# Performance work log

Measured on AMD Instinct MI355X. Metric: run time of the kernel, lower is better.

The kernel has to match this reference:

```python
import jax, jax.numpy as jnp
import numpy as np
import math

D_MODEL = 1024
N_HEADS = 16
D_FF = 4096
EPS = 1e-6
NEG = -1e9


def layer_norm(x, gamma, beta):
    # Faithful to torch: std with Bessel correction (ddof=1), eps added to std.
    mean = jnp.mean(x, axis=-1, keepdims=True)
    std = jnp.std(x, axis=-1, keepdims=True, ddof=1)
    return gamma * ((x - mean) / (std + EPS)) + beta


def mha(x_q, x_kv, wq, bq, wk, bk, wv, bv, wo, bo, mask):
    B, Sq, D = x_q.shape
    Sk = x_kv.shape[1]
    dk = D // N_HEADS
    q = (x_q @ wq + bq).reshape(B, Sq, N_HEADS, dk).transpose(0, 2, 1, 3)
    k = (x_kv @ wk + bk).reshape(B, Sk, N_HEADS, dk).transpose(0, 2, 1, 3)
    v = (x_kv @ wv + bv).reshape(B, Sk, N_HEADS, dk).transpose(0, 2, 1, 3)
    scores = jnp.einsum('bhqd,bhkd->bhqk', q, k) / math.sqrt(dk)
    scores = jnp.where(mask == 0, NEG, scores)
    attn = jax.nn.softmax(scores, axis=-1)
    out = jnp.einsum('bhqk,bhkd->bhqd', attn, v)
    out = out.transpose(0, 2, 1, 3).reshape(B, Sq, D)
    return out @ wo + bo


def setup_inputs() -> dict:
    key = jax.random.key(0)
    ks = jax.random.split(key, 24)
    B, S, D = 2, 2048, D_MODEL
    sc = 0.02
    lin = lambda k, i, o: jax.random.normal(k, (i, o), jnp.float32) * sc
    inp = {
        'x': jax.random.normal(ks[0], (B, S, D), jnp.float32),
        'encoder_output': jax.random.normal(ks[1], (B, S, D), jnp.float32),
        'src_mask': jnp.ones((1, 1, 1, S), jnp.int32),
        'tgt_mask': jnp.tril(jnp.ones((S, S), jnp.int32))[None, None],
        # self-attention params
        'sa_wq': lin(ks[2], D, D), 'sa_bq': jnp.zeros((D,), jnp.float32),
        'sa_wk': lin(ks[3], D, D), 'sa_bk': jnp.zeros((D,), jnp.float32),
        'sa_wv': lin(ks[4], D, D), 'sa_bv': jnp.zeros((D,), jnp.float32),
        'sa_wo': lin(ks[5], D, D), 'sa_bo': jnp.zeros((D,), jnp.float32),
        # cross-attention params
        'ca_wq': lin(ks[6], D, D), 'ca_bq': jnp.zeros((D,), jnp.float32),
        'ca_wk': lin(ks[7], D, D), 'ca_bk': jnp.zeros((D,), jnp.float32),
        'ca_wv': lin(ks[8], D, D), 'ca_bv': jnp.zeros((D,), jnp.float32),
        'ca_wo': lin(ks[9], D, D), 'ca_bo': jnp.zeros((D,), jnp.float32),
        # feed-forward params
        'ff_w1': lin(ks[10], D, D_FF), 'ff_b1': jnp.zeros((D_FF,), jnp.float32),
        'ff_w2': lin(ks[11], D_FF, D), 'ff_b2': jnp.zeros((D,), jnp.float32),
        # layer norms (3 residual connections)
        'n1_g': jnp.ones((D,), jnp.float32), 'n1_b': jnp.zeros((D,), jnp.float32),
        'n2_g': jnp.ones((D,), jnp.float32), 'n2_b': jnp.zeros((D,), jnp.float32),
        'n3_g': jnp.ones((D,), jnp.float32), 'n3_b': jnp.zeros((D,), jnp.float32),
    }
    return inp


def reference(x, encoder_output, src_mask, tgt_mask,
              sa_wq, sa_bq, sa_wk, sa_bk, sa_wv, sa_bv, sa_wo, sa_bo,
              ca_wq, ca_bq, ca_wk, ca_bk, ca_wv, ca_bv, ca_wo, ca_bo,
              ff_w1, ff_b1, ff_w2, ff_b2,
              n1_g, n1_b, n2_g, n2_b, n3_g, n3_b):
    # Pre-norm residual block 1: self-attention (dropout=0 -> identity)
    h = layer_norm(x, n1_g, n1_b)
    x = x + mha(h, h, sa_wq, sa_bq, sa_wk, sa_bk, sa_wv, sa_bv, sa_wo, sa_bo, tgt_mask)
    # Block 2: cross-attention over encoder output
    h = layer_norm(x, n2_g, n2_b)
    x = x + mha(h, encoder_output, ca_wq, ca_bq, ca_wk, ca_bk, ca_wv, ca_bv, ca_wo, ca_bo, src_mask)
    # Block 3: feed-forward
    h = layer_norm(x, n3_g, n3_b)
    ff = jax.nn.relu(h @ ff_w1 + ff_b1) @ ff_w2 + ff_b2
    return x + ff
```

## Files before the change

### kernel.cpp

```cpp
#include <hip/hip_runtime.h>

typedef short short8 __attribute__((ext_vector_type(8)));
typedef float f32x4 __attribute__((ext_vector_type(4)));

#define SEQ 2048
#define QSCALE 0.18033688011112042f
#define PSHIFT 20.0f
#define EXP2(x) __builtin_amdgcn_exp2f(x)

#define GLDS(g, l) __builtin_amdgcn_global_load_lds( \
    (const __attribute__((address_space(1))) unsigned int*)(g), \
    (__attribute__((address_space(3))) unsigned int*)(l), 16, 0, 0)

__device__ __forceinline__ unsigned short f2bf(float f) {
    unsigned int u = __builtin_bit_cast(unsigned int, f);
    unsigned int r = (u + 0x7fffu + ((u >> 16) & 1u)) >> 16;
    return (unsigned short)r;
}

__global__ __launch_bounds__(256)
void wtrans8_kernel(const float* w0, const float* w1, const float* w2, const float* w3,
                    const float* w4, const float* w5, const float* w6, const float* w7,
                    unsigned short* __restrict__ outbase)
{
    const float* Ws[8] = {w0, w1, w2, w3, w4, w5, w6, w7};
    const float* __restrict__ W = Ws[blockIdx.z];
    unsigned short* __restrict__ Wt = outbase + (size_t)blockIdx.z * 1024 * 1024;
    __shared__ float t[32][33];
    const int tx = threadIdx.x & 31;
    const int ty = threadIdx.x >> 5;
    const int nb = blockIdx.x * 32;
    const int kb = blockIdx.y * 32;
#pragma unroll
    for (int i = 0; i < 4; i++)
        t[ty + i * 8][tx] = W[(size_t)(kb + ty + i * 8) * 1024 + nb + tx];
    __syncthreads();
#pragma unroll
    for (int i = 0; i < 4; i++)
        Wt[(size_t)(nb + ty + i * 8) * 1024 + kb + tx] = f2bf(t[tx][ty + i * 8]);
}

__global__ __launch_bounds__(256)
void wtrans_kernel(const float* __restrict__ W, unsigned short* __restrict__ Wt,
                   int Kd, int Nd)
{
    __shared__ float t[32][33];
    const int tx = threadIdx.x & 31;
    const int ty = threadIdx.x >> 5;
    const int nb = blockIdx.x * 32;
    const int kb = blockIdx.y * 32;
#pragma unroll
    for (int i = 0; i < 4; i++)
        t[ty + i * 8][tx] = W[(size_t)(kb + ty + i * 8) * Nd + nb + tx];
    __syncthreads();
#pragma unroll
    for (int i = 0; i < 4; i++)
        Wt[(size_t)(nb + ty + i * 8) * Kd + kb + tx] = f2bf(t[tx][ty + i * 8]);
}

__global__ __launch_bounds__(256)
void cvt_kernel(const float* __restrict__ in, unsigned short* __restrict__ out, int n)
{
    int i = (blockIdx.x * 256 + threadIdx.x) * 4;
    if (i < n) {
        float4 v = *(const float4*)(in + i);
        ushort4 o;
        o.x = f2bf(v.x); o.y = f2bf(v.y); o.z = f2bf(v.z); o.w = f2bf(v.w);
        *(ushort4*)(out + i) = o;
    }
}

__global__ __launch_bounds__(256)
void ln_kernel(const float* __restrict__ x, const float* __restrict__ g,
               const float* __restrict__ bb, unsigned short* __restrict__ out)
{
    const int D = 1024;
    const int row = blockIdx.x;
    const float* xr = x + (size_t)row * D;
    float v[4];
    float s = 0.f, ss = 0.f;
#pragma unroll
    for (int i = 0; i < 4; i++) {
        v[i] = xr[threadIdx.x + i * 256];
        s += v[i];
        ss += v[i] * v[i];
    }
#pragma unroll
    for (int off = 1; off < 64; off <<= 1) {
        s  += __shfl_xor(s,  off, 64);
        ss += __shfl_xor(ss, off, 64);
    }
    __shared__ float red[8];
    const int wave = threadIdx.x >> 6;
    if ((threadIdx.x & 63) == 0) { red[wave] = s; red[4 + wave] = ss; }
    __syncthreads();
    s  = red[0] + red[1] + red[2] + red[3];
    ss = red[4] + red[5] + red[6] + red[7];
    float mean = s / D;
    float var  = fmaxf((ss - s * mean) / (D - 1), 0.f);
    float inv  = 1.f / (sqrtf(var) + 1e-6f);
#pragma unroll
    for (int i = 0; i < 4; i++) {
        int c = threadIdx.x + i * 256;
        out[(size_t)row * D + c] = f2bf(g[c] * (v[i] - mean) * inv + bb[c]);
    }
}

template <int MODE>
__global__ __launch_bounds__(256)
void gemm_kernel(const unsigned short* __restrict__ A,
                 const unsigned short* __restrict__ A2,
                 const unsigned short* __restrict__ Wt,
                 const float* __restrict__ b0,
                 const float* __restrict__ b1,
                 const float* __restrict__ b2,
                 unsigned short* __restrict__ o0,
                 unsigned short* __restrict__ o1,
                 unsigned short* __restrict__ o2,
                 int M, int N, int K)
{
    __shared__ unsigned short As[128 * 32];
    __shared__ unsigned short Bs[128 * 32];
    const int tid  = threadIdx.x;
    const int lane = tid & 63;
    const int wv   = tid >> 6;
    const int quad = lane >> 4;
    const int l16  = lane & 15;
    const int m0 = blockIdx.y * 128;
    const int n0 = blockIdx.x * 128;
    const int wm = (wv >> 1) << 6;
    const int wn = (wv & 1) << 6;
    const int sect = (MODE == 1) ? (n0 >> 10) : 0;
    const unsigned short* Asel = (MODE == 1 && sect != 0) ? A2 : A;

    const int srow0 = wv * 32 + (lane >> 2);
    const int srow1 = srow0 + 16;
    const int scol8 = (lane & 3) * 8;
    unsigned short* asw0 = &As[(wv * 2 + 0) * 512];
    unsigned short* asw1 = &As[(wv * 2 + 1) * 512];
    unsigned short* bsw0 = &Bs[(wv * 2 + 0) * 512];
    unsigned short* bsw1 = &Bs[(wv * 2 + 1) * 512];
    const unsigned short* Ag0 = Asel + (size_t)(m0 + srow0) * K + scol8;
    const unsigned short* Ag1 = Asel + (size_t)(m0 + srow1) * K + scol8;
    const unsigned short* Bg0 = Wt   + (size_t)(n0 + srow0) * K + scol8;
    const unsigned short* Bg1 = Wt   + (size_t)(n0 + srow1) * K + scol8;

    f32x4 acc[4][4];
#pragma unroll
    for (int i = 0; i < 4; i++)
#pragma unroll
        for (int j = 0; j < 4; j++) acc[i][j] = f32x4{0.f, 0.f, 0.f, 0.f};

    for (int k0 = 0; k0 < K; k0 += 32) {
        GLDS(Ag0 + k0, asw0);
        GLDS(Ag1 + k0, asw1);
        GLDS(Bg0 + k0, bsw0);
        GLDS(Bg1 + k0, bsw1);
        __syncthreads();
        short8 af[4], bfr[4];
#pragma unroll
        for (int i = 0; i < 4; i++)
            af[i] = *(const short8*)(&As[(wm + i * 16 + l16) * 32 + quad * 8]);
#pragma unroll
        for (int i = 0; i < 4; i++)
            bfr[i] = *(const short8*)(&Bs[(wn + i * 16 + l16) * 32 + quad * 8]);
#pragma unroll
        for (int mi = 0; mi < 4; mi++)
#pragma unroll
            for (int ni = 0; ni < 4; ni++)
                acc[mi][ni] = __builtin_amdgcn_mfma_f32_16x16x32_bf16(
                    af[mi], bfr[ni], acc[mi][ni], 0, 0, 0);
        __syncthreads();
    }

    if (MODE == 1) {
        const float* bias = (sect == 0) ? b0 : ((sect == 1) ? b1 : b2);
        if (sect == 2) {
#pragma unroll
            for (int mi = 0; mi < 4; mi++)
#pragma unroll
                for (int ni = 0; ni < 4; ni++) {
                    const int cc = (n0 + wn + ni * 16 + l16) & 1023;
                    const int h = cc >> 6, d = cc & 63;
                    const float bv = bias[cc];
                    const int rowg = m0 + wm + mi * 16 + quad * 4;
                    const int b = rowg >> 11, s = rowg & 2047;
                    ushort4 o4;
                    o4.x = f2bf(acc[mi][ni][0] + bv);
                    o4.y = f2bf(acc[mi][ni][1] + bv);
                    o4.z = f2bf(acc[mi][ni][2] + bv);
                    o4.w = f2bf(acc[mi][ni][3] + bv);
                    *(ushort4*)&o2[((size_t)(b * 16 + h) * 64 + d) * SEQ + s] = o4;
                }
        } else {
            unsigned short* dst = (sect == 0) ? o0 : o1;
            const float scl = (sect == 0) ? QSCALE : 1.0f;
#pragma unroll
            for (int mi = 0; mi < 4; mi++)
#pragma unroll
                for (int ni = 0; ni < 4; ni++) {
                    const int cc = (n0 + wn + ni * 16 + l16) & 1023;
                    const int h = cc >> 6, d = cc & 63;
                    const float bv = bias[cc];
#pragma unroll
                    for (int r = 0; r < 4; r++) {
                        const int rowg = m0 + wm + mi * 16 + quad * 4 + r;
                        const int b = rowg >> 11, s = rowg & 2047;
                        float v = (acc[mi][ni][r] + bv) * scl;
                        dst[((size_t)(b * 16 + h) * SEQ + s) * 64 + d] = f2bf(v);
                    }
                }
        }
    } else {
#pragma unroll
        for (int mi = 0; mi < 4; mi++)
#pragma unroll
            for (int ni = 0; ni < 4; ni++) {
                const int colg = n0 + wn + ni * 16 + l16;
                const float bv = b0[colg];
#pragma unroll
                for (int r = 0; r < 4; r++) {
                    const int rowg = m0 + wm + mi * 16 + quad * 4 + r;
                    float v = acc[mi][ni][r] + bv;
                    o0[(size_t)rowg * N + colg] = f2bf(fmaxf(v, 0.f));
                }
            }
    }
}

__global__ __launch_bounds__(256, 1)
void gemm_db_kernel(const unsigned short* __restrict__ A,
                    const unsigned short* __restrict__ Wt,
                    const float* __restrict__ b0,
                    const float* __restrict__ res,
                    float* __restrict__ outf,
                    int M, int N, int K, int cm, int cn)
{
    __shared__ unsigned short As[2][128 * 64];
    __shared__ unsigned short Bs[2][128 * 64];
    const int tid  = threadIdx.x;
    const int lane = tid & 63;
    const int wv   = tid >> 6;
    const int quad = lane >> 4;
    const int l16  = lane & 15;
    const int NX  = gridDim.x;
    const int id  = blockIdx.y * NX + blockIdx.x;
    const int xcd = id & 7, slot = id >> 3;
    const int ngx = NX / cn;
    const int rg = xcd / ngx, cg = xcd - rg * ngx;
    const int m0 = (rg * cm + (slot % cm)) * 128;
    const int n0 = (cg * cn + (slot / cm)) * 128;
    const int wm = (wv >> 1) << 6;
    const int wn = (wv & 1) << 6;

    const int rsub = lane >> 3;
    const int cu8  = ((lane & 7) ^ rsub) * 8;
    const unsigned short* Ag = A  + (size_t)(m0 + wv * 32 + rsub) * K + cu8;
    const unsigned short* Bg = Wt + (size_t)(n0 + wv * 32 + rsub) * K + cu8;

    f32x4 acc[4][4];
#pragma unroll
    for (int i = 0; i < 4; i++)
#pragma unroll
        for (int j = 0; j < 4; j++) acc[i][j] = f32x4{0.f, 0.f, 0.f, 0.f};

    const int NT = K >> 6;

    short8 ar[4], br[4];

    auto ldregs = [&](int t) {
        const int kb = t << 6;
#pragma unroll
        for (int r = 0; r < 4; r++) {
            ar[r] = *(const short8*)(Ag + (size_t)(r * 8) * K + kb);
            br[r] = *(const short8*)(Bg + (size_t)(r * 8) * K + kb);
        }
    };
    auto wrlds = [&](int b) {
#pragma unroll
        for (int r = 0; r < 4; r++) {
            *(short8*)&As[b][(wv * 4 + r) * 512 + lane * 8] = ar[r];
            *(short8*)&Bs[b][(wv * 4 + r) * 512 + lane * 8] = br[r];
        }
    };

    ldregs(0);
    asm volatile("s_waitcnt vmcnt(0)" ::: "memory");
    wrlds(0);
    asm volatile("s_waitcnt lgkmcnt(0)" ::: "memory");
    __builtin_amdgcn_s_barrier();

    for (int i = 0; i < NT; i++) {
        const int cur = i & 1;
        if (i + 1 < NT) ldregs(i + 1);

#pragma unroll
        for (int ks = 0; ks < 2; ks++) {
            short8 af[4], bfr[4];
#pragma unroll
            for (int mi = 0; mi < 4; mi++)
                af[mi] = *(const short8*)(&As[cur][(wm + mi * 16 + l16) * 64 +
                             (((ks * 4 + quad) ^ (l16 & 7)) * 8)]);
#pragma unroll
            for (int ni = 0; ni < 4; ni++)
                bfr[ni] = *(const short8*)(&Bs[cur][(wn + ni * 16 + l16) * 64 +
                             (((ks * 4 + quad) ^ (l16 & 7)) * 8)]);
#pragma unroll
            for (int mi = 0; mi < 4; mi++)
#pragma unroll
                for (int ni = 0; ni < 4; ni++)
                    acc[mi][ni] = __builtin_amdgcn_mfma_f32_16x16x32_bf16(
                        af[mi], bfr[ni], acc[mi][ni], 0, 0, 0);
        }

        if (i + 1 < NT) {
            asm volatile("s_waitcnt vmcnt(0)" ::: "memory");
            wrlds(cur ^ 1);
            asm volatile("s_waitcnt lgkmcnt(0)" ::: "memory");
            __builtin_amdgcn_s_barrier();
        }
    }

#pragma unroll
    for (int mi = 0; mi < 4; mi++)
#pragma unroll
        for (int ni = 0; ni < 4; ni++) {
            const int colg = n0 + wn + ni * 16 + l16;
            const float bv = b0[colg];
#pragma unroll
            for (int r = 0; r < 4; r++) {
                const int rowg = m0 + wm + mi * 16 + quad * 4 + r;
                outf[(size_t)rowg * N + colg] =
                    acc[mi][ni][r] + bv + res[(size_t)rowg * N + colg];
            }
        }
}

template <bool CAUSAL>
__global__ __launch_bounds__(256, 2)
void attn4_kernel(const unsigned short* __restrict__ Q,
                  const unsigned short* __restrict__ K,
                  const unsigned short* __restrict__ VT,
                  unsigned short* __restrict__ O)
{
    __shared__ unsigned short Ks[128 * 72];
    __shared__ unsigned short Vt[64 * 136];
    __shared__ unsigned short Ps[4][32 * 136];
    __shared__ float sumS[4][32];
    const int tid  = threadIdx.x;
    const int lane = tid & 63;
    const int wave = tid >> 6;
    const int quad = lane >> 4;
    const int l16  = lane & 15;
    const int bh = blockIdx.y;
    const int qb = (CAUSAL && (bh & 16)) ? (15 - (int)blockIdx.x) : (int)blockIdx.x;
    const int q0 = qb * 128;
    const size_t baseK = (size_t)bh * SEQ * 64;
    const size_t baseV = (size_t)bh * 64 * SEQ;

    short8 aq[2][2];
#pragma unroll
    for (int qs = 0; qs < 2; qs++) {
        const unsigned short* qp =
            Q + baseK + (size_t)(q0 + wave * 32 + qs * 16 + l16) * 64 + quad * 8;
        aq[qs][0] = *(const short8*)(qp);
        aq[qs][1] = *(const short8*)(qp + 32);
    }
    f32x4 acc[4][2];
#pragma unroll
    for (int i = 0; i < 4; i++)
#pragma unroll
        for (int j = 0; j < 2; j++) acc[i][j] = f32x4{0.f, 0.f, 0.f, 0.f};
    float lsum[2][4] = {{0.f, 0.f, 0.f, 0.f}, {0.f, 0.f, 0.f, 0.f}};

    const int nkb = CAUSAL ? (qb + 1) : (SEQ / 128);
    const int krow = tid >> 1;
    const int kc   = (tid & 1) * 32;
    const int vrow = tid >> 2;
    const int vc   = (tid & 3) * 32;
    const unsigned short* kg = K  + baseK + (size_t)krow * 64 + kc;
    const unsigned short* vg = VT + baseV + (size_t)vrow * SEQ + vc;

    short8 kr0 = *(const short8*)(kg),      kr1 = *(const short8*)(kg + 8);
    short8 kr2 = *(const short8*)(kg + 16), kr3 = *(const short8*)(kg + 24);
    short8 vr0 = *(const short8*)(vg),      vr1 = *(const short8*)(vg + 8);
    short8 vr2 = *(const short8*)(vg + 16), vr3 = *(const short8*)(vg + 24);

    for (int kb = 0; kb < nkb; kb++) {
        __syncthreads();
        *(short8*)&Ks[krow * 72 + kc]      = kr0;
        *(short8*)&Ks[krow * 72 + kc + 8]  = kr1;
        *(short8*)&Ks[krow * 72 + kc + 16] = kr2;
        *(short8*)&Ks[krow * 72 + kc + 24] = kr3;
        *(short8*)&Vt[vrow * 136 + vc]      = vr0;
        *(short8*)&Vt[vrow * 136 + vc + 8]  = vr1;
        *(short8*)&Vt[vrow * 136 + vc + 16] = vr2;
        *(short8*)&Vt[vrow * 136 + vc + 24] = vr3;
        if (kb + 1 < nkb) {
            const unsigned short* kg2 = kg + (size_t)(kb + 1) * 128 * 64;
            const unsigned short* vg2 = vg + (size_t)(kb + 1) * 128;
            kr0 = *(const short8*)(kg2);      kr1 = *(const short8*)(kg2 + 8);
            kr2 = *(const short8*)(kg2 + 16); kr3 = *(const short8*)(kg2 + 24);
            vr0 = *(const short8*)(vg2);      vr1 = *(const short8*)(vg2 + 8);
            vr2 = *(const short8*)(vg2 + 16); vr3 = *(const short8*)(vg2 + 24);
        }
        __syncthreads();

        const bool maskTile = CAUSAL && (kb == nkb - 1);
#pragma unroll
        for (int qs = 0; qs < 2; qs++) {
            f32x4 scf[8];
#pragma unroll
            for (int nt = 0; nt < 8; nt++) {
                f32x4 z = f32x4{0.f, 0.f, 0.f, 0.f};
#pragma unroll
                for (int c = 0; c < 2; c++) {
                    short8 bk = *(const short8*)(&Ks[(nt * 16 + l16) * 72 + c * 32 + quad * 8]);
                    z = __builtin_amdgcn_mfma_f32_16x16x32_bf16(aq[qs][c], bk, z, 0, 0, 0);
                }
                scf[nt] = z;
            }
            if (maskTile) {
                const int qg = q0 + wave * 32 + qs * 16 + quad * 4;
                const int k0 = kb * 128;
#pragma unroll
                for (int nt = 0; nt < 8; nt++) {
                    const int kg_ = k0 + nt * 16 + l16;
#pragma unroll
                    for (int r = 0; r < 4; r++)
                        if (kg_ > qg + r) scf[nt][r] = -1e9f;
                }
            }
#pragma unroll
            for (int nt = 0; nt < 8; nt++)
#pragma unroll
                for (int r = 0; r < 4; r++) {
                    float pv = EXP2(scf[nt][r] - PSHIFT);
                    lsum[qs][r] += pv;
                    Ps[wave][(qs * 16 + quad * 4 + r) * 136 +
                             ((nt * 16 + l16) ^ (quad * 8))] = f2bf(pv);
                }
        }
        const int pswz = 8 * (quad ^ ((l16 >> 2) & 3));
#pragma unroll
        for (int c = 0; c < 4; c++) {
            short8 av[4];
#pragma unroll
            for (int mi = 0; mi < 4; mi++)
                av[mi] = *(const short8*)(&Vt[(mi * 16 + l16) * 136 + c * 32 + quad * 8]);
#pragma unroll
            for (int qs = 0; qs < 2; qs++) {
                short8 bp = *(const short8*)(&Ps[wave][(qs * 16 + l16) * 136 + c * 32 + pswz]);
#pragma unroll
                for (int mi = 0; mi < 4; mi++)
                    acc[mi][qs] = __builtin_amdgcn_mfma_f32_16x16x32_bf16(av[mi], bp, acc[mi][qs], 0, 0, 0);
            }
        }
    }
#pragma unroll
    for (int qs = 0; qs < 2; qs++)
#pragma unroll
        for (int r = 0; r < 4; r++) {
#pragma unroll
            for (int off = 1; off < 16; off <<= 1)
                lsum[qs][r] += __shfl_xor(lsum[qs][r], off, 64);
        }
    if (l16 == 0) {
#pragma unroll
        for (int qs = 0; qs < 2; qs++)
#pragma unroll
            for (int r = 0; r < 4; r++)
                sumS[wave][qs * 16 + quad * 4 + r] = lsum[qs][r];
    }
    __syncthreads();
    const int b = bh >> 4, h = bh & 15;
#pragma unroll
    for (int qs = 0; qs < 2; qs++) {
        const float rcpL = 1.f / sumS[wave][qs * 16 + l16];
        const int qg = q0 + wave * 32 + qs * 16 + l16;
#pragma unroll
        for (int mi = 0; mi < 4; mi++) {
            ushort4 o4;
            o4.x = f2bf(acc[mi][qs][0] * rcpL);
            o4.y = f2bf(acc[mi][qs][1] * rcpL);
            o4.z = f2bf(acc[mi][qs][2] * rcpL);
            o4.w = f2bf(acc[mi][qs][3] * rcpL);
            *(ushort4*)&O[(size_t)(b * SEQ + qg) * 1024 + h * 64 + mi * 16 + quad * 4] = o4;
        }
    }
}

extern "C" void kernel_launch(void* const* d_in, const int* in_sizes, int n_in,
                              void* d_out, int out_size, void* d_ws, size_t ws_size,
                              hipStream_t stream)
{
    (void)in_sizes; (void)n_in; (void)out_size; (void)ws_size;
    const int B = 2, S = SEQ, D = 1024, DFF = 4096;
    const int M = B * S;

    const float* x     = (const float*)d_in[0];
    const float* enc   = (const float*)d_in[1];
    const float* sa_wq = (const float*)d_in[4],  *sa_bq = (const float*)d_in[5];
    const float* sa_wk = (const float*)d_in[6],  *sa_bk = (const float*)d_in[7];
    const float* sa_wv = (const float*)d_in[8],  *sa_bv = (const float*)d_in[9];
    const float* sa_wo = (const float*)d_in[10], *sa_bo = (const float*)d_in[11];
    const float* ca_wq = (const float*)d_in[12], *ca_bq = (const float*)d_in[13];
    const float* ca_wk = (const float*)d_in[14], *ca_bk = (const float*)d_in[15];
    const float* ca_wv = (const float*)d_in[16], *ca_bv = (const float*)d_in[17];
    const float* ca_wo = (const float*)d_in[18], *ca_bo = (const float*)d_in[19];
    const float* ff_w1 = (const float*)d_in[20], *ff_b1 = (const float*)d_in[21];
    const float* ff_w2 = (const float*)d_in[22], *ff_b2 = (const float*)d_in[23];
    const float* n1_g  = (const float*)d_in[24], *n1_b = (const float*)d_in[25];
    const float* n2_g  = (const float*)d_in[26], *n2_b = (const float*)d_in[27];
    const float* n3_g  = (const float*)d_in[28], *n3_b = (const float*)d_in[29];
    float* out = (float*)d_out;

    char* p = (char*)d_ws;
    auto carve = [&](size_t bytes) -> char* {
        char* r = p;
        p += (bytes + 255) & ~(size_t)255;
        return r;
    };
    unsigned short* wt8     = (unsigned short*)carve((size_t)8 * D * D * 2);
    unsigned short* wt_sqkv = wt8;
    unsigned short* wt_sao  = wt8 + (size_t)3 * D * D;
    unsigned short* wt_cqkv = wt8 + (size_t)4 * D * D;
    unsigned short* wt_cao  = wt8 + (size_t)7 * D * D;
    unsigned short* wt_ff1  = (unsigned short*)carve((size_t)D * DFF * 2);
    unsigned short* wt_ff2  = (unsigned short*)carve((size_t)DFF * D * 2);
    unsigned short* encb    = (unsigned short*)carve((size_t)M * D * 2);
    unsigned short* hb      = (unsigned short*)carve((size_t)M * D * 2);
    unsigned short* qbuf    = (unsigned short*)carve((size_t)M * D * 2);
    unsigned short* kbuf    = (unsigned short*)carve((size_t)M * D * 2);
    unsigned short* vtbuf   = (unsigned short*)carve((size_t)M * D * 2);
    unsigned short* ffh     = (unsigned short*)carve((size_t)M * DFF * 2);
    float* x1 = (float*)carve((size_t)M * D * 4);
    unsigned short* abuf = hb;
    float* x2 = out;

    dim3 blk(256);
    wtrans8_kernel<<<dim3(32, 32, 8), blk, 0, stream>>>(
        sa_wq, sa_wk, sa_wv, sa_wo, ca_wq, ca_wk, ca_wv, ca_wo, wt8);
    wtrans_kernel<<<dim3(DFF / 32, D / 32), blk, 0, stream>>>(ff_w1, wt_ff1, D, DFF);
    wtrans_kernel<<<dim3(D / 32, DFF / 32), blk, 0, stream>>>(ff_w2, wt_ff2, DFF, D);
    cvt_kernel<<<dim3(M * D / 1024), blk, 0, stream>>>(enc, encb, M * D);

    ln_kernel<<<dim3(M), blk, 0, stream>>>(x, n1_g, n1_b, hb);
    gemm_kernel<1><<<dim3(3 * D / 128, M / 128), blk, 0, stream>>>(
        hb, hb, wt_sqkv, sa_bq, sa_bk, sa_bv, qbuf, kbuf, vtbuf, M, 3 * D, D);
    attn4_kernel<true><<<dim3(S / 128, B * 16), blk, 0, stream>>>(qbuf, kbuf, vtbuf, abuf);
    gemm_db_kernel<<<dim3(D / 128, M / 128), blk, 0, stream>>>(
        abuf, wt_sao, sa_bo, x, x1, M, D, D, 8, 4);

    ln_kernel<<<dim3(M), blk, 0, stream>>>(x1, n2_g, n2_b, hb);
    gemm_kernel<1><<<dim3(3 * D / 128, M / 128), blk, 0, stream>>>(
        hb, encb, wt_cqkv, ca_bq, ca_bk, ca_bv, qbuf, kbuf, vtbuf, M, 3 * D, D);
    attn4_kernel<false><<<dim3(S / 128, B * 16), blk, 0, stream>>>(qbuf, kbuf, vtbuf, abuf);
    gemm_db_kernel<<<dim3(D / 128, M / 128), blk, 0, stream>>>(
        abuf, wt_cao, ca_bo, x1, x2, M, D, D, 8, 4);

    ln_kernel<<<dim3(M), blk, 0, stream>>>(x2, n3_g, n3_b, hb);
    gemm_kernel<2><<<dim3(DFF / 128, M / 128), blk, 0, stream>>>(
        hb, hb, wt_ff1, ff_b1, nullptr, nullptr, ffh, nullptr, nullptr, M, DFF, D);
    gemm_db_kernel<<<dim3(D / 128, M / 128), blk, 0, stream>>>(
        ffh, wt_ff2, ff_b2, x2, out, M, D, DFF, 4, 8);
}
```

Before: 582.2 us.

## Double-buffer QKV/FF1 GEMM through registers with XOR-swizzled LDS and BK=64

Replaces the single-buffered global_load_lds GEMM with a register-staged, double-buffered pipeline. The next K tile is loaded into registers while MFMAs run on the current LDS buffer. K tile doubles to 64, and the LDS layout is XOR-swizzled to avoid bank conflicts. The aim is to hide global latency and halve the barriers per K, at the cost of 64KB of LDS and launch_bounds(256,1), which may reduce occupancy.

```diff
diff --git a/kernel.cpp b/kernel.cpp
--- a/kernel.cpp
+++ b/kernel.cpp
@@ -7,10 +7,6 @@
 #define QSCALE 0.18033688011112042f
 #define PSHIFT 20.0f
 #define EXP2(x) __builtin_amdgcn_exp2f(x)
-
-#define GLDS(g, l) __builtin_amdgcn_global_load_lds( \
-    (const __attribute__((address_space(1))) unsigned int*)(g), \
-    (__attribute__((address_space(3))) unsigned int*)(l), 16, 0, 0)
 
 __device__ __forceinline__ unsigned short f2bf(float f) {
     unsigned int u = __builtin_bit_cast(unsigned int, f);
@@ -107,20 +103,20 @@
 }
 
 template <int MODE>
-__global__ __launch_bounds__(256)
-void gemm_kernel(const unsigned short* __restrict__ A,
-                 const unsigned short* __restrict__ A2,
-                 const unsigned short* __restrict__ Wt,
-                 const float* __restrict__ b0,
-                 const float* __restrict__ b1,
-                 const float* __restrict__ b2,
-                 unsigned short* __restrict__ o0,
-                 unsigned short* __restrict__ o1,
-                 unsigned short* __restrict__ o2,
-                 int M, int N, int K)
-{
-    __shared__ unsigned short As[128 * 32];
-    __shared__ unsigned short Bs[128 * 32];
+__global__ __launch_bounds__(256, 1)
+void gemm_rs_kernel(const unsigned short* __restrict__ A,
+                    const unsigned short* __restrict__ A2,
+                    const unsigned short* __restrict__ Wt,
+                    const float* __restrict__ b0,
+                    const float* __restrict__ b1,
+                    const float* __restrict__ b2,
+                    unsigned short* __restrict__ o0,
+                    unsigned short* __restrict__ o1,
+                    unsigned short* __restrict__ o2,
+                    int M, int N, int K)
+{
+    __shared__ unsigned short As[2][128 * 64];
+    __shared__ unsigned short Bs[2][128 * 64];
     const int tid  = threadIdx.x;
     const int lane = tid & 63;
     const int wv   = tid >> 6;
@@ -133,17 +129,10 @@
     const int sect = (MODE == 1) ? (n0 >> 10) : 0;
     const unsigned short* Asel = (MODE == 1 && sect != 0) ? A2 : A;
 
-    const int srow0 = wv * 32 + (lane >> 2);
-    const int srow1 = srow0 + 16;
-    const int scol8 = (lane & 3) * 8;
-    unsigned short* asw0 = &As[(wv * 2 + 0) * 512];
-    unsigned short* asw1 = &As[(wv * 2 + 1) * 512];
-    unsigned short* bsw0 = &Bs[(wv * 2 + 0) * 512];
-    unsigned short* bsw1 = &Bs[(wv * 2 + 1) * 512];
-    const unsigned short* Ag0 = Asel + (size_t)(m0 + srow0) * K + scol8;
-    const unsigned short* Ag1 = Asel + (size_t)(m0 + srow1) * K + scol8;
-    const unsigned short* Bg0 = Wt   + (size_t)(n0 + srow0) * K + scol8;
-    const unsigned short* Bg1 = Wt   + (size_t)(n0 + srow1) * K + scol8;
+    const int rsub = lane >> 3;
+    const int cu8  = ((lane & 7) ^ rsub) * 8;
+    const unsigned short* Ag = Asel + (size_t)(m0 + wv * 32 + rsub) * K + cu8;
+    const unsigned short* Bg = Wt   + (size_t)(n0 + wv * 32 + rsub) * K + cu8;
 
     f32x4 acc[4][4];
 #pragma unroll
@@ -151,26 +140,61 @@
 #pragma unroll
         for (int j = 0; j < 4; j++) acc[i][j] = f32x4{0.f, 0.f, 0.f, 0.f};
 
-    for (int k0 = 0; k0 < K; k0 += 32) {
-        GLDS(Ag0 + k0, asw0);
-        GLDS(Ag1 + k0, asw1);
-        GLDS(Bg0 + k0, bsw0);
-        GLDS(Bg1 + k0, bsw1);
-        __syncthreads();
-        short8 af[4], bfr[4];
-#pragma unroll
-        for (int i = 0; i < 4; i++)
-            af[i] = *(const short8*)(&As[(wm + i * 16 + l16) * 32 + quad * 8]);
-#pragma unroll
-        for (int i = 0; i < 4; i++)
-            bfr[i] = *(const short8*)(&Bs[(wn + i * 16 + l16) * 32 + quad * 8]);
-#pragma unroll
-        for (int mi = 0; mi < 4; mi++)
+    const int NT = K >> 6;
+
+    short8 ar[4], br[4];
+
+    auto ldregs = [&](int t) {
+        const int kb = t << 6;
+#pragma unroll
+        for (int r = 0; r < 4; r++) {
+            ar[r] = *(const short8*)(Ag + (size_t)(r * 8) * K + kb);
+            br[r] = *(const short8*)(Bg + (size_t)(r * 8) * K + kb);
+        }
+    };
+    auto wrlds = [&](int b) {
+#pragma unroll
+        for (int r = 0; r < 4; r++) {
+            *(short8*)&As[b][(wv * 4 + r) * 512 + lane * 8] = ar[r];
+            *(short8*)&Bs[b][(wv * 4 + r) * 512 + lane * 8] = br[r];
+        }
+    };
+
+    ldregs(0);
+    asm volatile("s_waitcnt vmcnt(0)" ::: "memory");
+    wrlds(0);
+    asm volatile("s_waitcnt lgkmcnt(0)" ::: "memory");
+    __builtin_amdgcn_s_barrier();
+
+    for (int i = 0; i < NT; i++) {
+        const int cur = i & 1;
+        if (i + 1 < NT) ldregs(i + 1);
+
+#pragma unroll
+        for (int ks = 0; ks < 2; ks++) {
+            short8 af[4], bfr[4];
+#pragma unroll
+            for (int mi = 0; mi < 4; mi++)
+                af[mi] = *(const short8*)(&As[cur][(wm + mi * 16 + l16) * 64 +
+                             (((ks * 4 + quad) ^ (l16 & 7)) * 8)]);
 #pragma unroll
             for (int ni = 0; ni < 4; ni++)
-                acc[mi][ni] = __builtin_amdgcn_mfma_f32_16x16x32_bf16(
-                    af[mi], bfr[ni], acc[mi][ni], 0, 0, 0);
-        __syncthreads();
+                bfr[ni] = *(const short8*)(&Bs[cur][(wn + ni * 16 + l16) * 64 +
+                             (((ks * 4 + quad) ^ (l16 & 7)) * 8)]);
+#pragma unroll
+            for (int mi = 0; mi < 4; mi++)
+#pragma unroll
+                for (int ni = 0; ni < 4; ni++)
+                    acc[mi][ni] = __builtin_amdgcn_mfma_f32_16x16x32_bf16(
+                        af[mi], bfr[ni], acc[mi][ni], 0, 0, 0);
+        }
+
+        if (i + 1 < NT) {
+            asm volatile("s_waitcnt vmcnt(0)" ::: "memory");
+            wrlds(cur ^ 1);
+            asm volatile("s_waitcnt lgkmcnt(0)" ::: "memory");
+            __builtin_amdgcn_s_barrier();
+        }
     }
 
     if (MODE == 1) {
@@ -546,21 +570,21 @@
     cvt_kernel<<<dim3(M * D / 1024), blk, 0, stream>>>(enc, encb, M * D);
 
     ln_kernel<<<dim3(M), blk, 0, stream>>>(x, n1_g, n1_b, hb);
-    gemm_kernel<1><<<dim3(3 * D / 128, M / 128), blk, 0, stream>>>(
+    gemm_rs_kernel<1><<<dim3(3 * D / 128, M / 128), blk, 0, stream>>>(
         hb, hb, wt_sqkv, sa_bq, sa_bk, sa_bv, qbuf, kbuf, vtbuf, M, 3 * D, D);
     attn4_kernel<true><<<dim3(S / 128, B * 16), blk, 0, stream>>>(qbuf, kbuf, vtbuf, abuf);
     gemm_db_kernel<<<dim3(D / 128, M / 128), blk, 0, stream>>>(
         abuf, wt_sao, sa_bo, x, x1, M, D, D, 8, 4);
 
     ln_kernel<<<dim3(M), blk, 0, stream>>>(x1, n2_g, n2_b, hb);
-    gemm_kernel<1><<<dim3(3 * D / 128, M / 128), blk, 0, stream>>>(
+    gemm_rs_kernel<1><<<dim3(3 * D / 128, M / 128), blk, 0, stream>>>(
         hb, encb, wt_cqkv, ca_bq, ca_bk, ca_bv, qbuf, kbuf, vtbuf, M, 3 * D, D);
     attn4_kernel<false><<<dim3(S / 128, B * 16), blk, 0, stream>>>(qbuf, kbuf, vtbuf, abuf);
     gemm_db_kernel<<<dim3(D / 128, M / 128), blk, 0, stream>>>(
         abuf, wt_cao, ca_bo, x1, x2, M, D, D, 8, 4);
 
     ln_kernel<<<dim3(M), blk, 0, stream>>>(x2, n3_g, n3_b, hb);
-    gemm_kernel<2><<<dim3(DFF / 128, M / 128), blk, 0, stream>>>(
+    gemm_rs_kernel<2><<<dim3(DFF / 128, M / 128), blk, 0, stream>>>(
         hb, hb, wt_ff1, ff_b1, nullptr, nullptr, ffh, nullptr, nullptr, M, DFF, D);
     gemm_db_kernel<<<dim3(D / 128, M / 128), blk, 0, stream>>>(
         ffh, wt_ff2, ff_b2, x2, out, M, D, DFF, 4, 8);
```

Result: faster. 534.7 us (-8.1%).
